# Kernel tuning notes

Measured on AMD Instinct MI355X. Metric: run time of the kernel, lower is better.

Reference implementation:

```python
import jax, jax.numpy as jnp
import numpy as np

N, F_IN, F_OUT, K, B = 4096, 64, 64, 5, 8
NAN_FRAC = 0.1


def ex_relu(mean, var):
    # E[ReLU(X)] for X ~ N(mean, var); where var==0 this is relu(mean).
    std = jnp.sqrt(jnp.maximum(var, 0.0))
    safe_std = jnp.where(std > 0, std, 1.0)
    z = mean / safe_std
    pdf = jnp.exp(-0.5 * z * z) / jnp.sqrt(2.0 * jnp.pi)
    cdf = 0.5 * (1.0 + jax.lax.erf(z / jnp.sqrt(2.0)))
    ex = mean * cdf + std * pdf
    return jnp.where(std > 0, ex, jnp.maximum(mean, 0.0))


def setup_inputs() -> dict:
    key = jax.random.key(0)
    ks = jax.random.split(key, 8)
    shift = jax.random.normal(ks[0], (N, N), dtype=jnp.float32) / jnp.sqrt(N)
    A2 = jax.random.uniform(ks[1], (N, N), dtype=jnp.float32) / N
    features = jax.random.normal(ks[2], (B, N, F_IN), dtype=jnp.float32)
    nan_mask = jax.random.bernoulli(ks[3], NAN_FRAC, (B, N, F_IN))
    features = jnp.where(nan_mask, jnp.nan, features)
    weight = jax.random.normal(ks[4], (F_IN, F_OUT), dtype=jnp.float32) * jnp.sqrt(2.0 / (F_IN + F_OUT))
    pi = jax.nn.log_softmax(jax.random.normal(ks[5], (K,), dtype=jnp.float32))
    mu = jax.random.normal(ks[6], (K, F_IN), dtype=jnp.float32)
    sigma = jax.random.normal(ks[7], (K, F_IN), dtype=jnp.float32) * 0.1  # log diag covariances
    return {"shift": shift, "A2": A2, "features": features,
            "weight": weight, "pi": pi, "mu": mu, "sigma": sigma}


def reference(shift, A2, features, weight, pi, mu, sigma):
    var = jnp.exp(sigma)                                    # [K,F]
    isnan = jnp.isnan(features)[:, None]                    # [B,1,N,F]
    feat_b = jnp.where(jnp.isnan(features), 0.0, features)[:, None]  # NaN-sanitized [B,1,N,F]
    mean_mat = jnp.where(isnan, mu[None, :, None, :], feat_b)        # [B,K,N,F]
    var_mat = jnp.where(isnan, var[None, :, None, :], 0.0)           # [B,K,N,F]
    # masked feature transform
    tx = jnp.einsum('bknf,fo->bkno', mean_mat, weight)       # [B,K,N,O]
    tc = jnp.einsum('bknf,fo->bkno', var_mat, weight * weight)
    # per-component graph conv (spmm)
    cx = jnp.einsum('nm,bkmo->bkno', shift, tx)
    cc = jnp.einsum('nm,bkmo->bkno', A2, tc)
    ex = ex_relu(cx, cc)                                     # [B,K,N,O]
    # responsibilities
    f_dim = features.shape[-1]
    log_n = (-0.5 * jnp.sum((mean_mat - mu[None, :, None, :]) ** 2 / var[None, :, None, :], axis=-1)
             - 0.5 * f_dim * jnp.log(2.0 * jnp.pi) - 0.5 * jnp.sum(sigma))  # [B,K,N]
    gamma = jax.nn.softmax(pi[None, :, None] + log_n, axis=1)               # softmax over components
    return jnp.sum(ex * gamma[..., None], axis=1)            # [B,N,O]
```

## Files before the change

kernel.cpp:

```cpp
#include <hip/hip_runtime.h>

#define NN 4096
#define FF 64
#define OO 64
#define KK 5
#define BB 8

typedef unsigned short bf16_t;
typedef __attribute__((ext_vector_type(8))) short short8;
typedef __attribute__((ext_vector_type(4))) float floatx4;

__device__ __forceinline__ unsigned short f2bf(float x) {
  unsigned int u = __float_as_uint(x);
  return (unsigned short)((u + 0x7fffu + ((u >> 16) & 1u)) >> 16);
}
__device__ __forceinline__ bool is_nan(float x) {
  return (__float_as_uint(x) & 0x7fffffffu) > 0x7f800000u;
}
__device__ __forceinline__ void gld16(const void* g, void* l) {
  __builtin_amdgcn_global_load_lds(
      (__attribute__((address_space(1))) const unsigned int*)g,
      (__attribute__((address_space(3))) unsigned int*)l, 16, 0, 0);
}

__global__ __launch_bounds__(256) void prep_kernel(
    const float* __restrict__ W, const float* __restrict__ sigma, const float* __restrict__ mu,
    float* __restrict__ ivarr, bf16_t* __restrict__ WTb,
    bf16_t* __restrict__ EkT, bf16_t* __restrict__ DkT) {
  int t = blockIdx.x * 256 + threadIdx.x;
  if (t < KK * FF) ivarr[t] = expf(-sigma[t]);
  if (t < FF * OO) {
    int o = t >> 6, f = t & 63;
    WTb[t] = f2bf(W[f * OO + o]);
  }
  int k = t >> 12, o = (t >> 6) & 63, f = t & 63;
  if (k < KK) {
    float w = W[f * OO + o];
    EkT[t] = f2bf(mu[k * FF + f] * w);
    DkT[t] = f2bf(expf(sigma[k * FF + f]) * w * w);
  }
}

__global__ __launch_bounds__(256) void cast2_kernel(
    const float* __restrict__ s0, const float* __restrict__ s1,
    bf16_t* __restrict__ d0, bf16_t* __restrict__ d1) {
  int i = (blockIdx.x * 256 + threadIdx.x) * 8;
  if (i + 8 > NN * NN) return;
  float4 a = *(const float4*)(s0 + i);
  float4 b = *(const float4*)(s0 + i + 4);
  union { unsigned short h[8]; uint4 v; } r;
  r.h[0] = f2bf(a.x); r.h[1] = f2bf(a.y); r.h[2] = f2bf(a.z); r.h[3] = f2bf(a.w);
  r.h[4] = f2bf(b.x); r.h[5] = f2bf(b.y); r.h[6] = f2bf(b.z); r.h[7] = f2bf(b.w);
  *(uint4*)(d0 + i) = r.v;
  a = *(const float4*)(s1 + i);
  b = *(const float4*)(s1 + i + 4);
  r.h[0] = f2bf(a.x); r.h[1] = f2bf(a.y); r.h[2] = f2bf(a.z); r.h[3] = f2bf(a.w);
  r.h[4] = f2bf(b.x); r.h[5] = f2bf(b.y); r.h[6] = f2bf(b.z); r.h[7] = f2bf(b.w);
  *(uint4*)(d1 + i) = r.v;
}

__global__ __launch_bounds__(256) void stage1_kernel(
    const float* __restrict__ feat, const float* __restrict__ pi,
    const float* __restrict__ mu, const float* __restrict__ ivarr,
    bf16_t* __restrict__ BigBT, bf16_t* __restrict__ MT2, float* __restrict__ gamma) {
  __shared__ bf16_t F0s[64][72];
  __shared__ bf16_t Ms[64][72];
  int t = threadIdx.x;
  int b = blockIdx.x >> 6;
  int n0 = (blockIdx.x & 63) << 6;
  int r = t >> 2, c4 = t & 3;
  const float* frow = feat + ((size_t)b * NN + n0 + r) * FF + c4 * 16;

  float s[KK] = {0.f, 0.f, 0.f, 0.f, 0.f};
#pragma unroll
  for (int ch = 0; ch < 4; ++ch) {
    float4 v4 = *(const float4*)(frow + ch * 4);
    float vv[4] = {v4.x, v4.y, v4.z, v4.w};
#pragma unroll
    for (int e = 0; e < 4; ++e) {
      int f = c4 * 16 + ch * 4 + e;
      bool nb = is_nan(vv[e]);
      float x = nb ? 0.f : vv[e];
      F0s[r][f] = nb ? (bf16_t)0 : f2bf(x);
      Ms[r][f] = nb ? (bf16_t)0x3F80 : (bf16_t)0;
#pragma unroll
      for (int k = 0; k < KK; ++k) {
        float d = nb ? 0.f : (x - mu[k * FF + f]);
        s[k] = fmaf(d * d, ivarr[k * FF + f], s[k]);
      }
    }
  }
#pragma unroll
  for (int k = 0; k < KK; ++k) {
    s[k] += __shfl_xor(s[k], 1);
    s[k] += __shfl_xor(s[k], 2);
  }
  if (c4 == 0) {
    float l[KK], mx = -3.0e38f;
#pragma unroll
    for (int k = 0; k < KK; ++k) { l[k] = pi[k] - 0.5f * s[k]; mx = fmaxf(mx, l[k]); }
    float ek[KK], sum = 0.f;
#pragma unroll
    for (int k = 0; k < KK; ++k) { ek[k] = expf(l[k] - mx); sum += ek[k]; }
    float inv = 1.0f / sum;
#pragma unroll
    for (int k = 0; k < KK; ++k)
      gamma[((size_t)(b * KK + k)) * NN + n0 + r] = ek[k] * inv;
  }
  __syncthreads();
  int f = t >> 2, nc = t & 3;
  union { bf16_t h[8]; uint4 v; } p;
#pragma unroll
  for (int half = 0; half < 2; ++half) {
    int nb8 = nc * 16 + half * 8;
#pragma unroll
    for (int e = 0; e < 8; ++e) p.h[e] = F0s[nb8 + e][f];
    *(uint4*)(BigBT + ((size_t)(b * 128 + f)) * NN + n0 + nb8) = p.v;
  }
#pragma unroll
  for (int half = 0; half < 2; ++half) {
    int nb8 = nc * 16 + half * 8;
#pragma unroll
    for (int e = 0; e < 8; ++e) p.h[e] = Ms[nb8 + e][f];
    *(uint4*)(BigBT + ((size_t)(b * 128 + 64 + f)) * NN + n0 + nb8) = p.v;
    *(uint4*)(MT2 + ((size_t)(b * 64 + f)) * NN + n0 + nb8) = p.v;
  }
}

__global__ __launch_bounds__(256) void gemm_bt_kernel(
    const bf16_t* __restrict__ A0, const bf16_t* __restrict__ B0, bf16_t* __restrict__ C0,
    const bf16_t* __restrict__ A1, const bf16_t* __restrict__ B1, bf16_t* __restrict__ C1) {
  __shared__ bf16_t As[128 * 64];
  __shared__ bf16_t Bs[128 * 64];
  int bid = blockIdx.x;
  const bf16_t *A, *B;
  bf16_t* C;
  int tile_m, tile_c, Cld;
  if (bid < 256) {
    A = A0; B = B0; C = C0; tile_m = bid >> 3; tile_c = bid & 7; Cld = 1024;
  } else {
    int b2 = bid - 256;
    A = A1; B = B1; C = C1; tile_m = b2 >> 2; tile_c = b2 & 3; Cld = 512;
  }

  int tid = threadIdx.x;
  int wave = tid >> 6, lane = tid & 63;
  int wm = wave >> 1, wc = wave & 1;

  int srow = wave * 32 + (lane >> 3);
  int scol = (((lane & 7) ^ (lane >> 3)) << 3);
  const bf16_t* Ag = A + (size_t)(tile_m * 128 + srow) * NN + scol;
  const bf16_t* Bg = B + (size_t)(tile_c * 128 + srow) * NN + scol;
  bf16_t* AsW = &As[(wave * 32) * 64];
  bf16_t* BsW = &Bs[(wave * 32) * 64];

  floatx4 acc[4][4];
#pragma unroll
  for (int i = 0; i < 4; ++i)
#pragma unroll
    for (int j = 0; j < 4; ++j) acc[i][j] = (floatx4){0.f, 0.f, 0.f, 0.f};

  int ml = lane & 15;
  int q = lane >> 4;
  int sw = ml & 7;

#pragma unroll 1
  for (int kt = 0; kt < 64; ++kt) {
    int k0 = kt * 64;
    __syncthreads();
#pragma unroll
    for (int i = 0; i < 4; ++i) {
      gld16(Ag + (size_t)(i * 8) * NN + k0, AsW + (i * 8) * 64);
      gld16(Bg + (size_t)(i * 8) * NN + k0, BsW + (i * 8) * 64);
    }
    __syncthreads();
#pragma unroll
    for (int ks = 0; ks < 2; ++ks) {
      int chunk = (((ks * 4 + q) ^ sw) << 3);
      short8 a[4], bb[4];
#pragma unroll
      for (int i = 0; i < 4; ++i)
        a[i] = *(const short8*)&As[(wm * 64 + i * 16 + ml) * 64 + chunk];
#pragma unroll
      for (int j = 0; j < 4; ++j)
        bb[j] = *(const short8*)&Bs[(wc * 64 + j * 16 + ml) * 64 + chunk];
#pragma unroll
      for (int i = 0; i < 4; ++i)
#pragma unroll
        for (int j = 0; j < 4; ++j)
          acc[i][j] = __builtin_amdgcn_mfma_f32_16x16x32_bf16(a[i], bb[j], acc[i][j], 0, 0, 0);
    }
  }

  int colb = tile_c * 128 + wc * 64 + ml;
#pragma unroll
  for (int i = 0; i < 4; ++i) {
    int mrow = tile_m * 128 + wm * 64 + i * 16 + q * 4;
#pragma unroll
    for (int j = 0; j < 4; ++j)
#pragma unroll
      for (int r = 0; r < 4; ++r)
        C[(size_t)(mrow + r) * Cld + colb + j * 16] = f2bf(acc[i][j][r]);
  }
}

__global__ __launch_bounds__(256) void stage2_kernel(
    const bf16_t* __restrict__ QR, const bf16_t* __restrict__ P,
    const bf16_t* __restrict__ WTb, const bf16_t* __restrict__ EkT,
    const bf16_t* __restrict__ DkT, const float* __restrict__ gamma,
    float* __restrict__ out) {
  int t = threadIdx.x;
  int b = blockIdx.x >> 6;
  int n0 = (blockIdx.x & 63) << 6;
  int w = t >> 6, lane = t & 63, m = lane & 15, q = lane >> 4;
  int n = n0 + w * 16 + m;

  short8 Qf[2], Rf[2], Pf[2], wfr[4][2];
#pragma unroll
  for (int ks = 0; ks < 2; ++ks) {
    Qf[ks] = *(const short8*)(QR + (size_t)n * 1024 + b * 128 + ks * 32 + q * 8);
    Rf[ks] = *(const short8*)(QR + (size_t)n * 1024 + b * 128 + 64 + ks * 32 + q * 8);
    Pf[ks] = *(const short8*)(P + (size_t)n * 512 + b * 64 + ks * 32 + q * 8);
  }
#pragma unroll
  for (int ot = 0; ot < 4; ++ot)
#pragma unroll
    for (int ks = 0; ks < 2; ++ks)
      wfr[ot][ks] = *(const short8*)(WTb + (ot * 16 + m) * 64 + ks * 32 + q * 8);

  floatx4 z = (floatx4){0.f, 0.f, 0.f, 0.f};
  floatx4 QW[4], osum[4];
#pragma unroll
  for (int ot = 0; ot < 4; ++ot) {
    QW[ot] = __builtin_amdgcn_mfma_f32_16x16x32_bf16(Qf[0], wfr[ot][0], z, 0, 0, 0);
    QW[ot] = __builtin_amdgcn_mfma_f32_16x16x32_bf16(Qf[1], wfr[ot][1], QW[ot], 0, 0, 0);
    osum[ot] = z;
  }

#pragma unroll
  for (int k = 0; k < KK; ++k) {
    float4 g4 = *(const float4*)(gamma + ((size_t)(b * KK + k)) * NN + n0 + w * 16 + q * 4);
    float gg[4] = {g4.x, g4.y, g4.z, g4.w};
#pragma unroll
    for (int ot = 0; ot < 4; ++ot) {
      const bf16_t* ek = EkT + ((k * 64 + ot * 16 + m) * 64) + q * 8;
      const bf16_t* dk = DkT + ((k * 64 + ot * 16 + m) * 64) + q * 8;
      short8 e0 = *(const short8*)ek, e1 = *(const short8*)(ek + 32);
      short8 d0 = *(const short8*)dk, d1 = *(const short8*)(dk + 32);
      floatx4 cx4 = __builtin_amdgcn_mfma_f32_16x16x32_bf16(Rf[0], e0, QW[ot], 0, 0, 0);
      cx4 = __builtin_amdgcn_mfma_f32_16x16x32_bf16(Rf[1], e1, cx4, 0, 0, 0);
      floatx4 cc4 = __builtin_amdgcn_mfma_f32_16x16x32_bf16(Pf[0], d0, z, 0, 0, 0);
      cc4 = __builtin_amdgcn_mfma_f32_16x16x32_bf16(Pf[1], d1, cc4, 0, 0, 0);
#pragma unroll
      for (int r = 0; r < 4; ++r) {
        float mm = cx4[r];
        float v = cc4[r];
        float sd = sqrtf(fmaxf(v, 0.f));
        float zz = mm / (sd > 0.f ? sd : 1.f);
        float pdf = expf(-0.5f * zz * zz) * 0.3989422804014327f;
        float cdf = 0.5f * (1.f + erff(zz * 0.7071067811865476f));
        float ex = sd > 0.f ? fmaf(mm, cdf, sd * pdf) : fmaxf(mm, 0.f);
        osum[ot][r] = fmaf(gg[r], ex, osum[ot][r]);
      }
    }
  }

#pragma unroll
  for (int ot = 0; ot < 4; ++ot)
#pragma unroll
    for (int r = 0; r < 4; ++r)
      out[((size_t)b * NN + n0 + w * 16 + q * 4 + r) * OO + ot * 16 + m] = osum[ot][r];
}

extern "C" void kernel_launch(void* const* d_in, const int* in_sizes, int n_in,
                              void* d_out, int out_size, void* d_ws, size_t ws_size,
                              hipStream_t stream) {
  const float* shift = (const float*)d_in[0];
  const float* A2    = (const float*)d_in[1];
  const float* feat  = (const float*)d_in[2];
  const float* W     = (const float*)d_in[3];
  const float* pi    = (const float*)d_in[4];
  const float* mu    = (const float*)d_in[5];
  const float* sigma = (const float*)d_in[6];
  float* out = (float*)d_out;

  char* ws = (char*)d_ws;
  bf16_t* shift_bf = (bf16_t*)(ws + 0);
  bf16_t* A2_bf    = (bf16_t*)(ws + 33554432);
  bf16_t* BigBT    = (bf16_t*)(ws + 67108864);
  bf16_t* MT2      = (bf16_t*)(ws + 75497472);
  bf16_t* QR       = (bf16_t*)(ws + 79691776);
  bf16_t* Pm       = (bf16_t*)(ws + 88080384);
  float*  gam      = (float*) (ws + 92274688);
  float*  ivarr    = (float*) (ws + 92930048);
  bf16_t* WTb      = (bf16_t*)(ws + 92931328);
  bf16_t* EkT      = (bf16_t*)(ws + 92939520);
  bf16_t* DkT      = (bf16_t*)(ws + 92980480);

  prep_kernel<<<80, 256, 0, stream>>>(W, sigma, mu, ivarr, WTb, EkT, DkT);
  cast2_kernel<<<8192, 256, 0, stream>>>(shift, A2, shift_bf, A2_bf);
  stage1_kernel<<<512, 256, 0, stream>>>(feat, pi, mu, ivarr, BigBT, MT2, gam);
  gemm_bt_kernel<<<384, 256, 0, stream>>>(shift_bf, BigBT, QR, A2_bf, MT2, Pm);
  stage2_kernel<<<512, 256, 0, stream>>>(QR, Pm, WTb, EkT, DkT, gam, out);
}
```

Before: 305.6 us.

## Split GEMM reduction dimension in two and sum partials in stage2

The graph-conv GEMM now splits the K dimension into two halves, doubling the grid from 384 to 768 blocks so more CUs are busy. Each half writes a separate bf16 partial, and stage2 adds the two partials when it loads its fragments. The separate MT2 buffer is dropped; the P GEMM reads the mask rows directly from BigBT through remapped row indices. Stage1's transpose write pattern and LDS padding are also changed. The cost is twice the partial-output writes and reads, plus an extra bf16 rounding step.

```diff
diff --git a/kernel.cpp b/kernel.cpp
--- a/kernel.cpp
+++ b/kernel.cpp
@@ -14,6 +14,9 @@
   unsigned int u = __float_as_uint(x);
   return (unsigned short)((u + 0x7fffu + ((u >> 16) & 1u)) >> 16);
 }
+__device__ __forceinline__ float bf2f(unsigned short h) {
+  return __uint_as_float(((unsigned int)h) << 16);
+}
 __device__ __forceinline__ bool is_nan(float x) {
   return (__float_as_uint(x) & 0x7fffffffu) > 0x7f800000u;
 }
@@ -21,6 +24,17 @@
   __builtin_amdgcn_global_load_lds(
       (__attribute__((address_space(1))) const unsigned int*)g,
       (__attribute__((address_space(3))) unsigned int*)l, 16, 0, 0);
+}
+
+union S8 { short8 s; int4 i; uint4 u; };
+
+__device__ __forceinline__ short8 addbf(short8 x, short8 y) {
+  S8 a, b, r;
+  a.s = x; b.s = y;
+#pragma unroll
+  for (int e = 0; e < 8; ++e)
+    r.s[e] = (short)f2bf(bf2f((unsigned short)a.s[e]) + bf2f((unsigned short)b.s[e]));
+  return r.s;
 }
 
 __global__ __launch_bounds__(256) void prep_kernel(
@@ -62,9 +76,9 @@
 __global__ __launch_bounds__(256) void stage1_kernel(
     const float* __restrict__ feat, const float* __restrict__ pi,
     const float* __restrict__ mu, const float* __restrict__ ivarr,
-    bf16_t* __restrict__ BigBT, bf16_t* __restrict__ MT2, float* __restrict__ gamma) {
-  __shared__ bf16_t F0s[64][72];
-  __shared__ bf16_t Ms[64][72];
+    bf16_t* __restrict__ BigBT, float* __restrict__ gamma) {
+  __shared__ bf16_t F0s[64][66];
+  __shared__ bf16_t Ms[64][66];
   int t = threadIdx.x;
   int b = blockIdx.x >> 6;
   int n0 = (blockIdx.x & 63) << 6;
@@ -108,39 +122,41 @@
       gamma[((size_t)(b * KK + k)) * NN + n0 + r] = ek[k] * inv;
   }
   __syncthreads();
-  int f = t >> 2, nc = t & 3;
-  union { bf16_t h[8]; uint4 v; } p;
-#pragma unroll
-  for (int half = 0; half < 2; ++half) {
-    int nb8 = nc * 16 + half * 8;
-#pragma unroll
-    for (int e = 0; e < 8; ++e) p.h[e] = F0s[nb8 + e][f];
-    *(uint4*)(BigBT + ((size_t)(b * 128 + f)) * NN + n0 + nb8) = p.v;
-  }
-#pragma unroll
-  for (int half = 0; half < 2; ++half) {
-    int nb8 = nc * 16 + half * 8;
-#pragma unroll
-    for (int e = 0; e < 8; ++e) p.h[e] = Ms[nb8 + e][f];
-    *(uint4*)(BigBT + ((size_t)(b * 128 + 64 + f)) * NN + n0 + nb8) = p.v;
-    *(uint4*)(MT2 + ((size_t)(b * 64 + f)) * NN + n0 + nb8) = p.v;
+#pragma unroll
+  for (int it = 0; it < 2; ++it) {
+    int f = it * 32 + (t >> 3);
+    int nc = t & 7;
+    union { bf16_t h[8]; uint4 v; } p;
+#pragma unroll
+    for (int e = 0; e < 8; ++e) p.h[e] = F0s[nc * 8 + e][f];
+    *(uint4*)(BigBT + ((size_t)(b * 128 + f)) * NN + n0 + nc * 8) = p.v;
+#pragma unroll
+    for (int e = 0; e < 8; ++e) p.h[e] = Ms[nc * 8 + e][f];
+    *(uint4*)(BigBT + ((size_t)(b * 128 + 64 + f)) * NN + n0 + nc * 8) = p.v;
   }
 }
 
 __global__ __launch_bounds__(256) void gemm_bt_kernel(
-    const bf16_t* __restrict__ A0, const bf16_t* __restrict__ B0, bf16_t* __restrict__ C0,
-    const bf16_t* __restrict__ A1, const bf16_t* __restrict__ B1, bf16_t* __restrict__ C1) {
+    const bf16_t* __restrict__ A0, const bf16_t* __restrict__ BigBT, bf16_t* __restrict__ C0,
+    const bf16_t* __restrict__ A1, bf16_t* __restrict__ C1) {
   __shared__ bf16_t As[128 * 64];
   __shared__ bf16_t Bs[128 * 64];
   int bid = blockIdx.x;
-  const bf16_t *A, *B;
+  const bf16_t* A;
   bf16_t* C;
-  int tile_m, tile_c, Cld;
-  if (bid < 256) {
-    A = A0; B = B0; C = C0; tile_m = bid >> 3; tile_c = bid & 7; Cld = 1024;
+  int tile_m, tile_c, kh, Cld;
+  bool isP;
+  if (bid < 512) {
+    isP = false; A = A0;
+    kh = bid & 1; int tmp = bid >> 1;
+    tile_m = tmp >> 3; tile_c = tmp & 7; Cld = 1024;
+    C = C0 + (size_t)kh * (NN * 1024);
   } else {
-    int b2 = bid - 256;
-    A = A1; B = B1; C = C1; tile_m = b2 >> 2; tile_c = b2 & 3; Cld = 512;
+    isP = true; A = A1;
+    int b2 = bid - 512;
+    kh = b2 & 1; int tmp = b2 >> 1;
+    tile_m = tmp >> 2; tile_c = tmp & 3; Cld = 512;
+    C = C1 + (size_t)kh * (NN * 512);
   }
 
   int tid = threadIdx.x;
@@ -150,7 +166,14 @@
   int srow = wave * 32 + (lane >> 3);
   int scol = (((lane & 7) ^ (lane >> 3)) << 3);
   const bf16_t* Ag = A + (size_t)(tile_m * 128 + srow) * NN + scol;
-  const bf16_t* Bg = B + (size_t)(tile_c * 128 + srow) * NN + scol;
+  int browi;
+  if (!isP) {
+    browi = tile_c * 128 + srow;
+  } else {
+    int c2 = tile_c * 128 + srow;
+    browi = ((c2 >> 6) << 7) + 64 + (c2 & 63);
+  }
+  const bf16_t* Bg = BigBT + (size_t)browi * NN + scol;
   bf16_t* AsW = &As[(wave * 32) * 64];
   bf16_t* BsW = &Bs[(wave * 32) * 64];
 
@@ -165,7 +188,7 @@
   int sw = ml & 7;
 
 #pragma unroll 1
-  for (int kt = 0; kt < 64; ++kt) {
+  for (int kt = kh * 32; kt < kh * 32 + 32; ++kt) {
     int k0 = kt * 64;
     __syncthreads();
 #pragma unroll
@@ -205,10 +228,12 @@
 }
 
 __global__ __launch_bounds__(256) void stage2_kernel(
-    const bf16_t* __restrict__ QR, const bf16_t* __restrict__ P,
+    const bf16_t* __restrict__ QRp, const bf16_t* __restrict__ Pp,
     const bf16_t* __restrict__ WTb, const bf16_t* __restrict__ EkT,
     const bf16_t* __restrict__ DkT, const float* __restrict__ gamma,
     float* __restrict__ out) {
+  const bf16_t* QR1 = QRp + (size_t)NN * 1024;
+  const bf16_t* Pp1 = Pp + (size_t)NN * 512;
   int t = threadIdx.x;
   int b = blockIdx.x >> 6;
   int n0 = (blockIdx.x & 63) << 6;
@@ -218,9 +243,11 @@
   short8 Qf[2], Rf[2], Pf[2], wfr[4][2];
 #pragma unroll
   for (int ks = 0; ks < 2; ++ks) {
-    Qf[ks] = *(const short8*)(QR + (size_t)n * 1024 + b * 128 + ks * 32 + q * 8);
-    Rf[ks] = *(const short8*)(QR + (size_t)n * 1024 + b * 128 + 64 + ks * 32 + q * 8);
-    Pf[ks] = *(const short8*)(P + (size_t)n * 512 + b * 64 + ks * 32 + q * 8);
+    size_t oq = (size_t)n * 1024 + b * 128 + ks * 32 + q * 8;
+    size_t op = (size_t)n * 512 + b * 64 + ks * 32 + q * 8;
+    Qf[ks] = addbf(*(const short8*)(QRp + oq), *(const short8*)(QR1 + oq));
+    Rf[ks] = addbf(*(const short8*)(QRp + oq + 64), *(const short8*)(QR1 + oq + 64));
+    Pf[ks] = addbf(*(const short8*)(Pp + op), *(const short8*)(Pp1 + op));
   }
 #pragma unroll
   for (int ot = 0; ot < 4; ++ot)
@@ -288,18 +315,17 @@
   bf16_t* shift_bf = (bf16_t*)(ws + 0);
   bf16_t* A2_bf    = (bf16_t*)(ws + 33554432);
   bf16_t* BigBT    = (bf16_t*)(ws + 67108864);
-  bf16_t* MT2      = (bf16_t*)(ws + 75497472);
-  bf16_t* QR       = (bf16_t*)(ws + 79691776);
-  bf16_t* Pm       = (bf16_t*)(ws + 88080384);
-  float*  gam      = (float*) (ws + 92274688);
-  float*  ivarr    = (float*) (ws + 92930048);
-  bf16_t* WTb      = (bf16_t*)(ws + 92931328);
-  bf16_t* EkT      = (bf16_t*)(ws + 92939520);
-  bf16_t* DkT      = (bf16_t*)(ws + 92980480);
+  bf16_t* QRp      = (bf16_t*)(ws + 75497472);
+  bf16_t* Pp       = (bf16_t*)(ws + 92274688);
+  float*  gam      = (float*) (ws + 100663296);
+  float*  ivarr    = (float*) (ws + 101318656);
+  bf16_t* WTb      = (bf16_t*)(ws + 101319936);
+  bf16_t* EkT      = (bf16_t*)(ws + 101328128);
+  bf16_t* DkT      = (bf16_t*)(ws + 101369088);
 
   prep_kernel<<<80, 256, 0, stream>>>(W, sigma, mu, ivarr, WTb, EkT, DkT);
   cast2_kernel<<<8192, 256, 0, stream>>>(shift, A2, shift_bf, A2_bf);
-  stage1_kernel<<<512, 256, 0, stream>>>(feat, pi, mu, ivarr, BigBT, MT2, gam);
-  gemm_bt_kernel<<<384, 256, 0, stream>>>(shift_bf, BigBT, QR, A2_bf, MT2, Pm);
-  stage2_kernel<<<512, 256, 0, stream>>>(QR, Pm, WTb, EkT, DkT, gam, out);
-}
+  stage1_kernel<<<512, 256, 0, stream>>>(feat, pi, mu, ivarr, BigBT, gam);
+  gemm_bt_kernel<<<768, 256, 0, stream>>>(shift_bf, BigBT, QRp, A2_bf, Pp);
+  stage2_kernel<<<512, 256, 0, stream>>>(QRp, Pp, WTb, EkT, DkT, gam, out);
+}
```

After: 285.3 us. 1.07x faster.
